# Kernel tuning notes

Hardware: AMD Instinct MI355X
Metric: run time of the kernel (lower is better)

The kernel has to match this reference:

```python
import jax, jax.numpy as jnp
import numpy as np

N_FFT = 4096
HOP = 1024
HALF = N_FFT // 2  # 2048; also number of freq bins is HALF+1 = 2049


def _make_kernels():
    # Periodic hann window, matching torch.hann_window(N) default (periodic=True)
    n = np.arange(N_FFT, dtype=np.float32)
    window = 0.5 * (1.0 - np.cos(2.0 * np.pi * n / N_FFT))
    freqs = np.arange(HALF + 1, dtype=np.float32)[:, None]  # [K,1]
    omega = 2.0 * np.pi * freqs * n[None, :] / N_FFT        # [K, n_fft]
    scale = np.float32(1.0 / np.sqrt(N_FFT))                # normalized=True
    cos_k = (np.cos(omega) * window[None, :] * scale).astype(np.float32)
    sin_k = (-np.sin(omega) * window[None, :] * scale).astype(np.float32)
    return jnp.asarray(cos_k), jnp.asarray(sin_k)


def setup_inputs() -> dict:
    key = jax.random.key(0)
    x = jax.random.normal(key, (32, 1, 441000), dtype=jnp.float32)
    cos_kernel, sin_kernel = _make_kernels()  # each [2049, 4096]
    return {"x": x, "cos_kernel": cos_kernel, "sin_kernel": sin_kernel}


def reference(x, cos_kernel, sin_kernel):
    # center=True: reflect-pad half_n_fft on each side of the time axis
    xp = jnp.pad(x, ((0, 0), (0, 0), (HALF, HALF)), mode='reflect')  # [B,1,L]
    L = xp.shape[-1]
    num_frames = (L - N_FFT) // HOP + 1
    # Frame extraction (equivalent to stride-HOP conv1d with width-N_FFT kernels)
    idx = HOP * jnp.arange(num_frames)[:, None] + jnp.arange(N_FFT)[None, :]  # [F, n_fft]
    frames = xp[:, 0, :][:, idx]  # [B, F, n_fft]
    real = jnp.einsum('bfn,kn->bkf', frames, cos_kernel)  # [B, 2049, F]
    imag = jnp.einsum('bfn,kn->bkf', frames, sin_kernel)  # [B, 2049, F]
    return jnp.stack((real, imag), axis=-1)  # [B, 2049, F, 2]
```

## Files before the change

kernel.cpp:

```cpp
#include <hip/hip_runtime.h>
#include <math.h>

#define NFFT  4096
#define MHALF 2048
#define HOPSZ 1024
#define LX    441000
#define NB    32
#define NF    431
#define NK    2049
#define NFPB  8
#define FBLK  54
#define NWG3  (NB * FBLK)
#define CH3   (NWG3 / 8)

#define SW(A) ((A) ^ (((A) >> 4) & 0xF))
#define WAVESYNC() do { asm volatile("s_waitcnt lgkmcnt(0)" ::: "memory"); \
                        __builtin_amdgcn_sched_barrier(0); } while (0)

typedef __fp16 half2v __attribute__((ext_vector_type(2)));

__device__ __forceinline__ float2 cadd(float2 a, float2 b){ return make_float2(a.x+b.x, a.y+b.y); }
__device__ __forceinline__ float2 csub(float2 a, float2 b){ return make_float2(a.x-b.x, a.y-b.y); }
__device__ __forceinline__ float2 cmul(float2 a, float2 b){
  return make_float2(fmaf(a.x, b.x, -(a.y*b.y)), fmaf(a.x, b.y, a.y*b.x));
}
#define STH(ptr, idx, v) (ptr)[idx] = __builtin_amdgcn_cvt_pkrtz((v).x, (v).y)
__device__ __forceinline__ float2 ldh(const half2v* __restrict__ X, int idx) {
  half2v h = X[idx];
  return make_float2((float)h.x, (float)h.y);
}

constexpr float W32C[22] = {
  1.0f, 0.98078528040323f, 0.92387953251129f, 0.83146961230255f, 0.70710678118655f,
  0.55557023301960f, 0.38268343236509f, 0.19509032201613f, 0.0f, -0.19509032201613f,
  -0.38268343236509f, -0.55557023301960f, -0.70710678118655f, -0.83146961230255f,
  -0.92387953251129f, -0.98078528040323f, -1.0f, -0.98078528040323f,
  -0.92387953251129f, -0.83146961230255f, -0.70710678118655f, -0.55557023301960f };
constexpr float W32S[22] = {
  0.0f, 0.19509032201613f, 0.38268343236509f, 0.55557023301960f, 0.70710678118655f,
  0.83146961230255f, 0.92387953251129f, 0.98078528040323f, 1.0f, 0.98078528040323f,
  0.92387953251129f, 0.83146961230255f, 0.70710678118655f, 0.55557023301960f,
  0.38268343236509f, 0.19509032201613f, 0.0f, -0.19509032201613f,
  -0.38268343236509f, -0.55557023301960f, -0.70710678118655f, -0.83146961230255f };

template<int N> __device__ __forceinline__ float2 w32m(float2 z) {
  if constexpr (N == 0) { return z; }
  else if constexpr (N == 8) { return make_float2(z.y, -z.x); }
  else {
    constexpr float c = W32C[N];
    constexpr float s = W32S[N];
    return make_float2(fmaf(z.x, c, z.y * s), fmaf(z.y, c, -(z.x * s)));
  }
}

__global__ void stft_init(float* __restrict__ ws) {
  int i = blockIdx.x * blockDim.x + threadIdx.x;
  const double PI = 3.14159265358979323846;
  if (i < 4096) {
    double w = 0.5 * (1.0 - cos(2.0 * PI * (double)i / 4096.0)) * (1.0 / 64.0);
    ws[i] = (float)w;
  }
  if (i < 1024) {
    double a = -2.0 * PI * (double)i / 2048.0;
    ws[4096 + 2 * i]     = (float)cos(a);
    ws[4096 + 2 * i + 1] = (float)sin(a);
  }
  if (i < 2049) {
    double a = -2.0 * PI * (double)i / 4096.0;
    ws[6144 + 2 * i]     = (float)cos(a);
    ws[6144 + 2 * i + 1] = (float)sin(a);
  }
}

__device__ __forceinline__ void dft8(const float2* a, float2* B) {
  float2 t0 = cadd(a[0], a[4]), t1 = csub(a[0], a[4]);
  float2 t2 = cadd(a[2], a[6]), t3 = csub(a[2], a[6]);
  float2 t4 = cadd(a[1], a[5]), t5 = csub(a[1], a[5]);
  float2 t6 = cadd(a[3], a[7]), t7 = csub(a[3], a[7]);
  const float K = 0.70710678118654752f;
  float2 wt5  = make_float2(K * (t5.x + t5.y), K * (t5.y - t5.x));
  float2 w3t7 = make_float2(K * (t7.y - t7.x), -K * (t7.x + t7.y));
  float2 wt7  = make_float2(K * (t7.x + t7.y), K * (t7.y - t7.x));
  float2 w3t5 = make_float2(K * (t5.y - t5.x), -K * (t5.x + t5.y));
  float2 e0 = cadd(t0, t2), e1 = csub(t0, t2);
  float2 f0 = cadd(t4, t6), f1 = csub(t4, t6);
  B[0] = cadd(e0, f0);
  B[4] = csub(e0, f0);
  B[2] = make_float2(e1.x + f1.y, e1.y - f1.x);
  B[6] = make_float2(e1.x - f1.y, e1.y + f1.x);
  float2 g0 = make_float2(t1.x + t3.y, t1.y - t3.x);
  float2 g1 = make_float2(t1.x - t3.y, t1.y + t3.x);
  float2 h0 = cadd(wt5, w3t7);
  float2 h1 = cadd(wt7, w3t5);
  B[1] = cadd(g0, h0);
  B[5] = csub(g0, h0);
  B[3] = cadd(g1, h1);
  B[7] = csub(g1, h1);
}

template<int S>
__device__ __forceinline__ void bf8(half2v* __restrict__ X, int sxor,
                                    const float2* __restrict__ twg,
                                    int j, const float2* a) {
  const int q = j & (S - 1);
  const int t = j - q;
  float2 B[8];
  dft8(a, B);
  float2 w1 = twg[t];
  float2 w2 = cmul(w1, w1);
  float2 w3 = cmul(w2, w1);
  float2 w4 = cmul(w2, w2);
  float2 w5 = cmul(w3, w2);
  float2 w6 = cmul(w3, w3);
  float2 w7 = cmul(w4, w3);
  const int o = q + 8 * t;
  STH(X, SW(o) ^ sxor, B[0]);
  { float2 v = cmul(w1, B[1]); STH(X, SW(o + S)     ^ sxor, v); }
  { float2 v = cmul(w2, B[2]); STH(X, SW(o + 2 * S) ^ sxor, v); }
  { float2 v = cmul(w3, B[3]); STH(X, SW(o + 3 * S) ^ sxor, v); }
  { float2 v = cmul(w4, B[4]); STH(X, SW(o + 4 * S) ^ sxor, v); }
  { float2 v = cmul(w5, B[5]); STH(X, SW(o + 5 * S) ^ sxor, v); }
  { float2 v = cmul(w6, B[6]); STH(X, SW(o + 6 * S) ^ sxor, v); }
  { float2 v = cmul(w7, B[7]); STH(X, SW(o + 7 * S) ^ sxor, v); }
}

__device__ __forceinline__ void loadwin(float2 (*a)[8], const float* __restrict__ xb,
                                        int f, int l,
                                        const float2* __restrict__ winv,
                                        const float* __restrict__ win) {
  const int base = f * HOPSZ - MHALF;
  if (base >= 0 && base + NFFT <= LX) {
    const float2* xv = (const float2*)(xb + base);
#pragma unroll
    for (int r = 0; r < 4; ++r) {
      const int j = l + (r << 6);
#pragma unroll
      for (int m = 0; m < 8; ++m) {
        const int idx = j + (m << 8);
        float2 v = xv[idx];
        float2 w = winv[idx];
        a[r][m] = make_float2(v.x * w.x, v.y * w.y);
      }
    }
  } else {
#pragma unroll
    for (int r = 0; r < 4; ++r) {
      const int j = l + (r << 6);
#pragma unroll
      for (int m = 0; m < 8; ++m) {
        const int idx = j + (m << 8);
        int s0 = base + 2 * idx;
        int s1 = s0 + 1;
        s0 = (s0 < 0) ? -s0 : ((s0 >= LX) ? (2 * LX - 2 - s0) : s0);
        s1 = (s1 < 0) ? -s1 : ((s1 >= LX) ? (2 * LX - 2 - s1) : s1);
        a[r][m] = make_float2(xb[s0] * win[2 * idx], xb[s1] * win[2 * idx + 1]);
      }
    }
  }
}

#define VBLK(dd, slp, sx, V) do {                                     \
    float2 tt[8], BB[8];                                              \
    tt[0] = dd[8*(V)+0];                                              \
    tt[1] = w32m<1*(V)>(dd[8*(V)+1]);                                 \
    tt[2] = w32m<2*(V)>(dd[8*(V)+2]);                                 \
    tt[3] = w32m<3*(V)>(dd[8*(V)+3]);                                 \
    tt[4] = w32m<4*(V)>(dd[8*(V)+4]);                                 \
    tt[5] = w32m<5*(V)>(dd[8*(V)+5]);                                 \
    tt[6] = w32m<6*(V)>(dd[8*(V)+6]);                                 \
    tt[7] = w32m<7*(V)>(dd[8*(V)+7]);                                 \
    dft8(tt, BB);                                                     \
    STH(slp, SW(l + (((V) +  0) << 6)) ^ sx, BB[0]);                  \
    STH(slp, SW(l + (((V) +  4) << 6)) ^ sx, BB[1]);                  \
    STH(slp, SW(l + (((V) +  8) << 6)) ^ sx, BB[2]);                  \
    STH(slp, SW(l + (((V) + 12) << 6)) ^ sx, BB[3]);                  \
    STH(slp, SW(l + (((V) + 16) << 6)) ^ sx, BB[4]);                  \
    STH(slp, SW(l + (((V) + 20) << 6)) ^ sx, BB[5]);                  \
    STH(slp, SW(l + (((V) + 24) << 6)) ^ sx, BB[6]);                  \
    STH(slp, SW(l + (((V) + 28) << 6)) ^ sx, BB[7]);                  \
  } while (0)

#define DFT4PASS(dd) do {                                             \
    _Pragma("unroll")                                                 \
    for (int m1 = 0; m1 < 8; ++m1) {                                  \
      float2 p0 = dd[m1], p1 = dd[m1 + 8], p2 = dd[m1 + 16], p3 = dd[m1 + 24]; \
      float2 e0 = cadd(p0, p2), e1 = csub(p0, p2);                    \
      float2 o0 = cadd(p1, p3), o1 = csub(p1, p3);                    \
      dd[m1]      = cadd(e0, o0);                                     \
      dd[m1 + 8]  = make_float2(e1.x + o1.y, e1.y - o1.x);            \
      dd[m1 + 16] = csub(e0, o0);                                     \
      dd[m1 + 24] = make_float2(e1.x - o1.y, e1.y + o1.x);            \
    }                                                                 \
  } while (0)

__global__ __launch_bounds__(256, 2) void stft_fft(const float* __restrict__ x,
                                                   const float* __restrict__ ws,
                                                   float* __restrict__ out) {
  __shared__ half2v fbuf[NFPB * 2048];

  const int tid = threadIdx.x;
  const int wid = (blockIdx.x & 7) * CH3 + (blockIdx.x >> 3);
  const int b  = wid / FBLK;
  const int fb = wid - b * FBLK;
  const int f0 = fb * NFPB;
  const int wv = tid >> 6;
  const int l  = tid & 63;
  const int fA = f0 + 2 * wv;
  const int fB = fA + 1;
  const bool hasB = (fB < NF);

  const float*  win  = ws;
  const float2* winv = (const float2*)ws;
  const float2* twg  = (const float2*)(ws + 4096);
  const float2* tw4  = (const float2*)(ws + 6144);
  const float* xb = x + (size_t)b * LX;

  half2v* __restrict__ slA = &fbuf[(2 * wv) * 2048];
  half2v* __restrict__ slB = &fbuf[(2 * wv + 1) * 2048];
  const int sxA = (2 * wv) << 2;
  const int sxB = (2 * wv + 1) << 2;

  {
    float2 aA[4][8], aB[4][8];
    loadwin(aA, xb, fA, l, winv, win);
    if (hasB) loadwin(aB, xb, fB, l, winv, win);
#pragma unroll
    for (int r = 0; r < 4; ++r) {
      bf8<1>(slA, sxA, twg, l + (r << 6), aA[r]);
      if (hasB) bf8<1>(slB, sxB, twg, l + (r << 6), aB[r]);
    }
    WAVESYNC();

#pragma unroll
    for (int r = 0; r < 4; ++r) {
      const int j = l + (r << 6);
#pragma unroll
      for (int m = 0; m < 8; ++m) {
        aA[r][m] = ldh(slA, SW(j + (m << 8)) ^ sxA);
        if (hasB) aB[r][m] = ldh(slB, SW(j + (m << 8)) ^ sxB);
      }
    }
    WAVESYNC();
#pragma unroll
    for (int r = 0; r < 4; ++r) {
      bf8<8>(slA, sxA, twg, l + (r << 6), aA[r]);
      if (hasB) bf8<8>(slB, sxB, twg, l + (r << 6), aB[r]);
    }
    WAVESYNC();
  }

  {
    float2 dA[32], dB[32];
#pragma unroll
    for (int m = 0; m < 32; ++m) {
      dA[m] = ldh(slA, SW(l + (m << 6)) ^ sxA);
      if (hasB) dB[m] = ldh(slB, SW(l + (m << 6)) ^ sxB);
    }
    WAVESYNC();
    DFT4PASS(dA);
    VBLK(dA, slA, sxA, 0); VBLK(dA, slA, sxA, 1);
    VBLK(dA, slA, sxA, 2); VBLK(dA, slA, sxA, 3);
    if (hasB) {
      DFT4PASS(dB);
      VBLK(dB, slB, sxB, 0); VBLK(dB, slB, sxB, 1);
      VBLK(dB, slB, sxB, 2); VBLK(dB, slB, sxB, 3);
    }
  }
  __syncthreads();

  float2* __restrict__ op = (float2*)out;
  const size_t obB = (size_t)b * NK * NF;
  const int s  = tid & 7;
  const int kk = tid >> 3;
  const int fS = f0 + s;
  const bool act = (fS < NF);
  const half2v* __restrict__ sl2 = &fbuf[s * 2048];
  const int sx2 = s << 2;
#pragma unroll 4
  for (int it = 0; it < 32; ++it) {
    const int k  = kk + (it << 5);
    const int km = (2048 - k) & 2047;
    float2 zk = ldh(sl2, SW(k)  ^ sx2);
    float2 zm = ldh(sl2, SW(km) ^ sx2);
    float xex = 0.5f * (zk.x + zm.x);
    float xey = 0.5f * (zk.y - zm.y);
    float xox = 0.5f * (zk.y + zm.y);
    float xoy = 0.5f * (zm.x - zk.x);
    float2 w = tw4[k];
    float tx = w.x * xox - w.y * xoy;
    float ty = w.x * xoy + w.y * xox;
    if (act) {
      op[obB + (size_t)k * NF + fS]          = make_float2(xex + tx,  xey + ty);
      op[obB + (size_t)(2048 - k) * NF + fS] = make_float2(xex - tx, -xey + ty);
    }
  }
  if (tid < 8 && (f0 + tid) < NF) {
    const half2v* slt = &fbuf[tid * 2048];
    float2 zq = ldh(slt, SW(1024) ^ (tid << 2));
    op[obB + (size_t)1024 * NF + (f0 + tid)] = make_float2(zq.x, -zq.y);
  }
}

extern "C" void kernel_launch(void* const* d_in, const int* in_sizes, int n_in,
                              void* d_out, int out_size, void* d_ws, size_t ws_size,
                              hipStream_t stream) {
  const float* x = (const float*)d_in[0];
  float* ws = (float*)d_ws;
  float* out = (float*)d_out;
  stft_init<<<16, 256, 0, stream>>>(ws);
  stft_fft<<<NWG3, 256, 0, stream>>>(x, ws, out);
}
```

Baseline: 129.2 us.

## Shrink FFT workgroups to single wave processing two frames

Reorganizes the STFT kernel so each workgroup is one 64-thread wave handling two frames instead of four waves handling eight frames. This removes the block-wide barrier in favor of a wave-local LDS wait and increases the number of workgroups for finer scheduling. In exchange, the output store phase now writes only two adjacent frames per frequency bin, shrinking contiguous store segments and likely reducing write coalescing on a store-bound output.

```diff
diff --git a/kernel.cpp b/kernel.cpp
--- a/kernel.cpp
+++ b/kernel.cpp
@@ -8,10 +8,10 @@
 #define NB    32
 #define NF    431
 #define NK    2049
-#define NFPB  8
-#define FBLK  54
-#define NWG3  (NB * FBLK)
-#define CH3   (NWG3 / 8)
+#define NFPW  2
+#define FBLK2 216
+#define NWG4  (NB * FBLK2)
+#define CH4   (NWG4 / 8)
 
 #define SW(A) ((A) ^ (((A) >> 4) & 0xF))
 #define WAVESYNC() do { asm volatile("s_waitcnt lgkmcnt(0)" ::: "memory"); \
@@ -193,20 +193,19 @@
     }                                                                 \
   } while (0)
 
-__global__ __launch_bounds__(256, 2) void stft_fft(const float* __restrict__ x,
-                                                   const float* __restrict__ ws,
-                                                   float* __restrict__ out) {
-  __shared__ half2v fbuf[NFPB * 2048];
+__global__ __launch_bounds__(64) void stft_fft(const float* __restrict__ x,
+                                               const float* __restrict__ ws,
+                                               float* __restrict__ out) {
+  __shared__ half2v fbuf[NFPW * 2048];
 
   const int tid = threadIdx.x;
-  const int wid = (blockIdx.x & 7) * CH3 + (blockIdx.x >> 3);
-  const int b  = wid / FBLK;
-  const int fb = wid - b * FBLK;
-  const int f0 = fb * NFPB;
-  const int wv = tid >> 6;
-  const int l  = tid & 63;
-  const int fA = f0 + 2 * wv;
-  const int fB = fA + 1;
+  const int wid = (blockIdx.x & 7) * CH4 + (blockIdx.x >> 3);
+  const int b  = wid / FBLK2;
+  const int fb = wid - b * FBLK2;
+  const int f0 = fb * NFPW;
+  const int l  = tid;
+  const int fA = f0;
+  const int fB = f0 + 1;
   const bool hasB = (fB < NF);
 
   const float*  win  = ws;
@@ -215,10 +214,10 @@
   const float2* tw4  = (const float2*)(ws + 6144);
   const float* xb = x + (size_t)b * LX;
 
-  half2v* __restrict__ slA = &fbuf[(2 * wv) * 2048];
-  half2v* __restrict__ slB = &fbuf[(2 * wv + 1) * 2048];
-  const int sxA = (2 * wv) << 2;
-  const int sxB = (2 * wv + 1) << 2;
+  half2v* __restrict__ slA = &fbuf[0];
+  half2v* __restrict__ slB = &fbuf[2048];
+  const int sxA = 0;
+  const int sxB = 4;
 
   {
     float2 aA[4][8], aB[4][8];
@@ -265,13 +264,13 @@
       VBLK(dB, slB, sxB, 0); VBLK(dB, slB, sxB, 1);
       VBLK(dB, slB, sxB, 2); VBLK(dB, slB, sxB, 3);
     }
-  }
-  __syncthreads();
+    WAVESYNC();
+  }
 
   float2* __restrict__ op = (float2*)out;
   const size_t obB = (size_t)b * NK * NF;
-  const int s  = tid & 7;
-  const int kk = tid >> 3;
+  const int s  = tid & 1;
+  const int kk = tid >> 1;
   const int fS = f0 + s;
   const bool act = (fS < NF);
   const half2v* __restrict__ sl2 = &fbuf[s * 2048];
@@ -294,7 +293,7 @@
       op[obB + (size_t)(2048 - k) * NF + fS] = make_float2(xex - tx, -xey + ty);
     }
   }
-  if (tid < 8 && (f0 + tid) < NF) {
+  if (tid < 2 && (f0 + tid) < NF) {
     const half2v* slt = &fbuf[tid * 2048];
     float2 zq = ldh(slt, SW(1024) ^ (tid << 2));
     op[obB + (size_t)1024 * NF + (f0 + tid)] = make_float2(zq.x, -zq.y);
@@ -308,5 +307,5 @@
   float* ws = (float*)d_ws;
   float* out = (float*)d_out;
   stft_init<<<16, 256, 0, stream>>>(ws);
-  stft_fft<<<NWG3, 256, 0, stream>>>(x, ws, out);
-}
+  stft_fft<<<NWG4, 64, 0, stream>>>(x, ws, out);
+}
```

After: 179.3 us. 38.8% more time.

## Table-driven FFT twiddles, hoisted LDS swizzle indices, paired-frame float4 output stores

Applied to the files above, without the earlier changes.

Adds a precomputed table of twiddle powers 1..7 to the workspace init. The radix-8 butterflies now load these powers instead of building them with chained complex multiplies. LDS swizzle offsets are computed once per row and reused across strided accesses, cutting integer ALU work. The output stage assigns two adjacent frames per thread and writes them as one float4 instead of two float2 stores, aiming at fewer, wider global writes; because NF is odd, many of these float4 addresses are only 8-byte aligned.

```diff
diff --git a/kernel.cpp b/kernel.cpp
--- a/kernel.cpp
+++ b/kernel.cpp
@@ -69,6 +69,13 @@
     double a = -2.0 * PI * (double)i / 4096.0;
     ws[6144 + 2 * i]     = (float)cos(a);
     ws[6144 + 2 * i + 1] = (float)sin(a);
+  }
+  if (i < 1792) {
+    int p = (i >> 8) + 1;
+    int t = i & 255;
+    double a = -2.0 * PI * (double)(p * t) / 2048.0;
+    ws[10244 + 2 * i]     = (float)cos(a);
+    ws[10244 + 2 * i + 1] = (float)sin(a);
   }
 }
 
@@ -99,20 +106,20 @@
 }
 
 template<int S>
-__device__ __forceinline__ void bf8(half2v* __restrict__ X, int sxor,
-                                    const float2* __restrict__ twg,
-                                    int j, const float2* a) {
+__device__ __forceinline__ void bf8t(half2v* __restrict__ X, int sxor,
+                                     const float2* __restrict__ wt,
+                                     int j, const float2* a) {
   const int q = j & (S - 1);
   const int t = j - q;
+  float2 w1 = wt[t];
+  float2 w2 = wt[256 + t];
+  float2 w3 = wt[512 + t];
+  float2 w4 = wt[768 + t];
+  float2 w5 = wt[1024 + t];
+  float2 w6 = wt[1280 + t];
+  float2 w7 = wt[1536 + t];
   float2 B[8];
   dft8(a, B);
-  float2 w1 = twg[t];
-  float2 w2 = cmul(w1, w1);
-  float2 w3 = cmul(w2, w1);
-  float2 w4 = cmul(w2, w2);
-  float2 w5 = cmul(w3, w2);
-  float2 w6 = cmul(w3, w3);
-  float2 w7 = cmul(w4, w3);
   const int o = q + 8 * t;
   STH(X, SW(o) ^ sxor, B[0]);
   { float2 v = cmul(w1, B[1]); STH(X, SW(o + S)     ^ sxor, v); }
@@ -159,7 +166,7 @@
   }
 }
 
-#define VBLK(dd, slp, sx, V) do {                                     \
+#define VBLK(dd, slp, B3, V) do {                                     \
     float2 tt[8], BB[8];                                              \
     tt[0] = dd[8*(V)+0];                                              \
     tt[1] = w32m<1*(V)>(dd[8*(V)+1]);                                 \
@@ -170,14 +177,8 @@
     tt[6] = w32m<6*(V)>(dd[8*(V)+6]);                                 \
     tt[7] = w32m<7*(V)>(dd[8*(V)+7]);                                 \
     dft8(tt, BB);                                                     \
-    STH(slp, SW(l + (((V) +  0) << 6)) ^ sx, BB[0]);                  \
-    STH(slp, SW(l + (((V) +  4) << 6)) ^ sx, BB[1]);                  \
-    STH(slp, SW(l + (((V) +  8) << 6)) ^ sx, BB[2]);                  \
-    STH(slp, SW(l + (((V) + 12) << 6)) ^ sx, BB[3]);                  \
-    STH(slp, SW(l + (((V) + 16) << 6)) ^ sx, BB[4]);                  \
-    STH(slp, SW(l + (((V) + 20) << 6)) ^ sx, BB[5]);                  \
-    STH(slp, SW(l + (((V) + 24) << 6)) ^ sx, BB[6]);                  \
-    STH(slp, SW(l + (((V) + 28) << 6)) ^ sx, BB[7]);                  \
+    _Pragma("unroll")                                                 \
+    for (int u = 0; u < 8; ++u) STH(slp, B3[V] + (u << 8), BB[u]);    \
   } while (0)
 
 #define DFT4PASS(dd) do {                                             \
@@ -211,8 +212,8 @@
 
   const float*  win  = ws;
   const float2* winv = (const float2*)ws;
-  const float2* twg  = (const float2*)(ws + 4096);
   const float2* tw4  = (const float2*)(ws + 6144);
+  const float2* wt   = (const float2*)(ws + 10244);
   const float* xb = x + (size_t)b * LX;
 
   half2v* __restrict__ slA = &fbuf[(2 * wv) * 2048];
@@ -226,78 +227,102 @@
     if (hasB) loadwin(aB, xb, fB, l, winv, win);
 #pragma unroll
     for (int r = 0; r < 4; ++r) {
-      bf8<1>(slA, sxA, twg, l + (r << 6), aA[r]);
-      if (hasB) bf8<1>(slB, sxB, twg, l + (r << 6), aB[r]);
+      bf8t<1>(slA, sxA, wt, l + (r << 6), aA[r]);
+      if (hasB) bf8t<1>(slB, sxB, wt, l + (r << 6), aB[r]);
     }
     WAVESYNC();
 
 #pragma unroll
     for (int r = 0; r < 4; ++r) {
       const int j = l + (r << 6);
+      const int bA = SW(j) ^ sxA;
+      const int bB = SW(j) ^ sxB;
 #pragma unroll
       for (int m = 0; m < 8; ++m) {
-        aA[r][m] = ldh(slA, SW(j + (m << 8)) ^ sxA);
-        if (hasB) aB[r][m] = ldh(slB, SW(j + (m << 8)) ^ sxB);
+        aA[r][m] = ldh(slA, bA + (m << 8));
+        if (hasB) aB[r][m] = ldh(slB, bB + (m << 8));
       }
     }
     WAVESYNC();
 #pragma unroll
     for (int r = 0; r < 4; ++r) {
-      bf8<8>(slA, sxA, twg, l + (r << 6), aA[r]);
-      if (hasB) bf8<8>(slB, sxB, twg, l + (r << 6), aB[r]);
+      bf8t<8>(slA, sxA, wt, l + (r << 6), aA[r]);
+      if (hasB) bf8t<8>(slB, sxB, wt, l + (r << 6), aB[r]);
     }
     WAVESYNC();
   }
 
   {
+    int b3A[4], b3B[4];
+#pragma unroll
+    for (int v = 0; v < 4; ++v) {
+      const int sv = SW(l + (v << 6));
+      b3A[v] = sv ^ sxA;
+      b3B[v] = sv ^ sxB;
+    }
     float2 dA[32], dB[32];
 #pragma unroll
-    for (int m = 0; m < 32; ++m) {
-      dA[m] = ldh(slA, SW(l + (m << 6)) ^ sxA);
-      if (hasB) dB[m] = ldh(slB, SW(l + (m << 6)) ^ sxB);
-    }
+    for (int v = 0; v < 4; ++v)
+#pragma unroll
+      for (int mm = 0; mm < 8; ++mm) {
+        dA[v + 4 * mm] = ldh(slA, b3A[v] + (mm << 8));
+        if (hasB) dB[v + 4 * mm] = ldh(slB, b3B[v] + (mm << 8));
+      }
     WAVESYNC();
     DFT4PASS(dA);
-    VBLK(dA, slA, sxA, 0); VBLK(dA, slA, sxA, 1);
-    VBLK(dA, slA, sxA, 2); VBLK(dA, slA, sxA, 3);
+    VBLK(dA, slA, b3A, 0); VBLK(dA, slA, b3A, 1);
+    VBLK(dA, slA, b3A, 2); VBLK(dA, slA, b3A, 3);
     if (hasB) {
       DFT4PASS(dB);
-      VBLK(dB, slB, sxB, 0); VBLK(dB, slB, sxB, 1);
-      VBLK(dB, slB, sxB, 2); VBLK(dB, slB, sxB, 3);
+      VBLK(dB, slB, b3B, 0); VBLK(dB, slB, b3B, 1);
+      VBLK(dB, slB, b3B, 2); VBLK(dB, slB, b3B, 3);
     }
   }
   __syncthreads();
 
   float2* __restrict__ op = (float2*)out;
   const size_t obB = (size_t)b * NK * NF;
-  const int s  = tid & 7;
-  const int kk = tid >> 3;
-  const int fS = f0 + s;
-  const bool act = (fS < NF);
-  const half2v* __restrict__ sl2 = &fbuf[s * 2048];
-  const int sx2 = s << 2;
+  const int pp = tid & 3;
+  const int kk = tid >> 2;
+  const int fS = f0 + 2 * pp;
+  const bool full = (fS + 1 < NF);
+  const half2v* __restrict__ sA2 = &fbuf[(2 * pp) * 2048];
+  const half2v* __restrict__ sB2 = &fbuf[(2 * pp + 1) * 2048];
+  const int sxa2 = (2 * pp) << 2;
+  const int sxb2 = (2 * pp + 1) << 2;
 #pragma unroll 4
-  for (int it = 0; it < 32; ++it) {
-    const int k  = kk + (it << 5);
+  for (int it = 0; it < 16; ++it) {
+    const int k  = kk + (it << 6);
     const int km = (2048 - k) & 2047;
-    float2 zk = ldh(sl2, SW(k)  ^ sx2);
-    float2 zm = ldh(sl2, SW(km) ^ sx2);
-    float xex = 0.5f * (zk.x + zm.x);
-    float xey = 0.5f * (zk.y - zm.y);
-    float xox = 0.5f * (zk.y + zm.y);
-    float xoy = 0.5f * (zm.x - zk.x);
     float2 w = tw4[k];
-    float tx = w.x * xox - w.y * xoy;
-    float ty = w.x * xoy + w.y * xox;
-    if (act) {
-      op[obB + (size_t)k * NF + fS]          = make_float2(xex + tx,  xey + ty);
-      op[obB + (size_t)(2048 - k) * NF + fS] = make_float2(xex - tx, -xey + ty);
-    }
-  }
-  if (tid < 8 && (f0 + tid) < NF) {
-    const half2v* slt = &fbuf[tid * 2048];
-    float2 zq = ldh(slt, SW(1024) ^ (tid << 2));
-    op[obB + (size_t)1024 * NF + (f0 + tid)] = make_float2(zq.x, -zq.y);
+    float2 zkA = ldh(sA2, SW(k) ^ sxa2);
+    float2 zmA = ldh(sA2, SW(km) ^ sxa2);
+    float2 zkB = ldh(sB2, SW(k) ^ sxb2);
+    float2 zmB = ldh(sB2, SW(km) ^ sxb2);
+    float xexA = 0.5f * (zkA.x + zmA.x), xeyA = 0.5f * (zkA.y - zmA.y);
+    float xoxA = 0.5f * (zkA.y + zmA.y), xoyA = 0.5f * (zmA.x - zkA.x);
+    float txA = w.x * xoxA - w.y * xoyA, tyA = w.x * xoyA + w.y * xoxA;
+    float xexB = 0.5f * (zkB.x + zmB.x), xeyB = 0.5f * (zkB.y - zmB.y);
+    float xoxB = 0.5f * (zkB.y + zmB.y), xoyB = 0.5f * (zmB.x - zkB.x);
+    float txB = w.x * xoxB - w.y * xoyB, tyB = w.x * xoyB + w.y * xoxB;
+    float* p0 = (float*)&op[obB + (size_t)k * NF + fS];
+    float* p1 = (float*)&op[obB + (size_t)(2048 - k) * NF + fS];
+    if (full) {
+      *(float4*)p0 = make_float4(xexA + txA,  xeyA + tyA, xexB + txB,  xeyB + tyB);
+      *(float4*)p1 = make_float4(xexA - txA, -xeyA + tyA, xexB - txB, -xeyB + tyB);
+    } else {
+      *(float2*)p0 = make_float2(xexA + txA,  xeyA + tyA);
+      *(float2*)p1 = make_float2(xexA - txA, -xeyA + tyA);
+    }
+  }
+  if (tid < 4) {
+    const int pq = tid;
+    const int fq = f0 + 2 * pq;
+    float2 zA = ldh(&fbuf[(2 * pq) * 2048],     SW(1024) ^ ((2 * pq) << 2));
+    float2 zB = ldh(&fbuf[(2 * pq + 1) * 2048], SW(1024) ^ ((2 * pq + 1) << 2));
+    float* p = (float*)&op[obB + (size_t)1024 * NF + fq];
+    if (fq + 1 < NF) *(float4*)p = make_float4(zA.x, -zA.y, zB.x, -zB.y);
+    else             *(float2*)p = make_float2(zA.x, -zA.y);
   }
 }
 
```

After: 148.3 us. +14.8%, slower.
